# Kernel tuning notes

Measured on AMD Instinct MI355X. Metric: run time of the kernel, lower is better.

The kernel has to match this reference:

```python
import jax, jax.numpy as jnp
import numpy as np

N_NODES = 100000
N_EDGES = 1_600_000
D_IN = 128
D_OUT = 128


def setup_inputs() -> dict:
    key = jax.random.key(0)
    k1, k2, k3 = jax.random.split(key, 3)
    input_matrix = jax.random.normal(k1, (N_NODES, D_IN), dtype=jnp.float32)
    adjacency_coo_matrix = jax.random.randint(k2, (2, N_EDGES), 0, N_NODES, dtype=jnp.int64)
    # xavier-uniform-style init for the weight matrix
    limit = float(np.sqrt(6.0 / (D_IN + D_OUT)))
    weights_matrix = jax.random.uniform(k3, (D_IN, D_OUT), dtype=jnp.float32, minval=-limit, maxval=limit)
    return {
        "input_matrix": input_matrix,
        "adjacency_coo_matrix": adjacency_coo_matrix,
        "weights_matrix": weights_matrix,
    }


def reference(input_matrix, adjacency_coo_matrix, weights_matrix):
    # Edge-wise gathers (the irregular-access pattern from the torch code)
    src_idx = adjacency_coo_matrix[0]
    dst_idx = adjacency_coo_matrix[1]
    neighbors = input_matrix[dst_idx]  # [E, D_IN] gather of neighbor features
    # Mean-aggregate neighbor features onto each src node
    agg = jax.ops.segment_sum(neighbors, src_idx, num_segments=N_NODES)  # [N, D_IN]
    deg = jax.ops.segment_sum(jnp.ones((neighbors.shape[0],), dtype=input_matrix.dtype),
                              src_idx, num_segments=N_NODES)  # [N]
    mean_agg = agg / jnp.maximum(deg, 1.0)[:, None]
    # Linear transform with the layer weight matrix
    out = mean_agg @ weights_matrix  # [N, D_OUT]
    return out
```

## Files before the change

### kernel.cpp

```cpp
#include <hip/hip_runtime.h>

#define NN 100000
#define NE 1600000
#define DD 128
#define CAP 64
#define SLICE_N 12500
#define FILL_BLOCKS 1024
#define BPS (FILL_BLOCKS / 8)
#define GEMM_ROWS 128
#define GEMM_BLOCKS ((NN + GEMM_ROWS - 1) / GEMM_ROWS)

typedef __bf16 bf16x8 __attribute__((ext_vector_type(8)));
typedef float  f32x4  __attribute__((ext_vector_type(4)));

__device__ __forceinline__ unsigned int f2bf(float f) {
    unsigned int u = __float_as_uint(f);
    return (u + 0x7FFFu + ((u >> 16) & 1u)) >> 16;
}
__device__ __forceinline__ float bflo(unsigned int u) { return __uint_as_float(u << 16); }
__device__ __forceinline__ float bfhi(unsigned int u) { return __uint_as_float(u & 0xFFFF0000u); }

__global__ __launch_bounds__(256) void k_prep(const float* __restrict__ W,
                                              unsigned short* __restrict__ wtb,
                                              int* __restrict__ cnt)
{
    const int idx = blockIdx.x * 256 + (int)threadIdx.x;
    const int k = idx >> 7, n = idx & 127;
    wtb[n * DD + k] = (unsigned short)f2bf(W[idx]);
    int4* c4 = (int4*)cnt;
    for (int i = idx; i < NN / 4; i += DD * DD) c4[i] = make_int4(0, 0, 0, 0);
}

__global__ __launch_bounds__(256, 8) void k_fused(const int* __restrict__ adj,
                                                  int* __restrict__ cnt,
                                                  int* __restrict__ edge_dst,
                                                  const float* __restrict__ x,
                                                  const unsigned short* __restrict__ wtb,
                                                  unsigned short* __restrict__ y)
{
    if (blockIdx.x < FILL_BLOCKS) {
        const int slice = blockIdx.x & 7;
        const int w     = blockIdx.x >> 3;
        const int lo    = slice * SLICE_N;
        const uint4* src4 = (const uint4*)adj;
        const uint4* dst4 = (const uint4*)(adj + NE);
        const int ngroups = NE / 4;
        const int stride  = BPS * 256;

        #define PROC(s4, d4) do {                                                     \
            _Pragma("unroll")                                                         \
            for (int j = 0; j < 4; ++j) {                                             \
                const int s = (j==0)?(int)(s4).x:(j==1)?(int)(s4).y:                  \
                              (j==2)?(int)(s4).z:(int)(s4).w;                         \
                const int d = (j==0)?(int)(d4).x:(j==1)?(int)(d4).y:                  \
                              (j==2)?(int)(d4).z:(int)(d4).w;                         \
                if ((unsigned)(s - lo) < (unsigned)SLICE_N) {                         \
                    int slot = atomicAdd(&cnt[s], 1);                                 \
                    if (slot < CAP) edge_dst[(size_t)s * CAP + slot] = d;             \
                }                                                                     \
            }                                                                         \
        } while (0)

        int g = w * 256 + (int)threadIdx.x;
        for (; g + stride < ngroups; g += 2 * stride) {
            const uint4 sa = src4[g],          da = dst4[g];
            const uint4 sb = src4[g + stride], db = dst4[g + stride];
            PROC(sa, da);
            PROC(sb, db);
        }
        for (; g < ngroups; g += stride) {
            const uint4 s4 = src4[g], d4 = dst4[g];
            PROC(s4, d4);
        }
        #undef PROC
        return;
    }

    const int bid  = blockIdx.x - FILL_BLOCKS;
    const int wave = (int)threadIdx.x >> 6;
    const int lane = (int)threadIdx.x & 63;
    const int quad = lane >> 4;
    const int l16  = lane & 15;

    #pragma unroll 1
    for (int mt = 0; mt < 2; ++mt) {
        const int mbase = bid * GEMM_ROWS + wave * 32 + mt * 16;
        const int m = mbase + l16;

        bf16x8 a[4];
        if (m < NN) {
            const float* arow = x + (size_t)m * DD + quad * 8;
            #pragma unroll
            for (int ks = 0; ks < 4; ++ks) {
                const float4 f0 = *(const float4*)(arow + ks * 32);
                const float4 f1 = *(const float4*)(arow + ks * 32 + 4);
                uint4 p;
                p.x = f2bf(f0.x) | (f2bf(f0.y) << 16);
                p.y = f2bf(f0.z) | (f2bf(f0.w) << 16);
                p.z = f2bf(f1.x) | (f2bf(f1.y) << 16);
                p.w = f2bf(f1.z) | (f2bf(f1.w) << 16);
                a[ks] = __builtin_bit_cast(bf16x8, p);
            }
        } else {
            const uint4 z = make_uint4(0, 0, 0, 0);
            #pragma unroll
            for (int ks = 0; ks < 4; ++ks) a[ks] = __builtin_bit_cast(bf16x8, z);
        }

        #pragma unroll
        for (int nt = 0; nt < 8; ++nt) {
            f32x4 c = {0.f, 0.f, 0.f, 0.f};
            const unsigned short* bcol = wtb + (nt * 16 + l16) * DD + quad * 8;
            #pragma unroll
            for (int ks = 0; ks < 4; ++ks) {
                const bf16x8 b = __builtin_bit_cast(bf16x8, *(const uint4*)(bcol + ks * 32));
                c = __builtin_amdgcn_mfma_f32_16x16x32_bf16(a[ks], b, c, 0, 0, 0);
            }
            #pragma unroll
            for (int r = 0; r < 4; ++r) {
                const int row = mbase + quad * 4 + r;
                if (row < NN)
                    y[(size_t)row * DD + nt * 16 + l16] = (unsigned short)f2bf(c[r]);
            }
        }
    }
}

__global__ __launch_bounds__(256) void k_agg2(const unsigned short* __restrict__ y,
                                              const int* __restrict__ cnt,
                                              const int* __restrict__ edge_dst,
                                              float* __restrict__ out)
{
    const int n    = blockIdx.x * 4 + ((int)threadIdx.x >> 6);
    const int lane = (int)threadIdx.x & 63;
    const int eg   = lane >> 4;
    const int h    = lane & 15;
    int deg = cnt[n];
    if (deg > CAP) deg = CAP;
    const int* el = edge_dst + (size_t)n * CAP;

    float acc[8] = {0.f,0.f,0.f,0.f,0.f,0.f,0.f,0.f};

    #define ACC(p) do {                                         \
        acc[0] += bflo((p).x); acc[1] += bfhi((p).x);           \
        acc[2] += bflo((p).y); acc[3] += bfhi((p).y);           \
        acc[4] += bflo((p).z); acc[5] += bfhi((p).z);           \
        acc[6] += bflo((p).w); acc[7] += bfhi((p).w);           \
    } while (0)

    int i = eg;
    for (; i + 12 < deg; i += 16) {
        const int d0 = el[i];
        const int d1 = el[i + 4];
        const int d2 = el[i + 8];
        const int d3 = el[i + 12];
        const uint4 p0 = *(const uint4*)(y + (size_t)d0 * DD + h * 8);
        const uint4 p1 = *(const uint4*)(y + (size_t)d1 * DD + h * 8);
        const uint4 p2 = *(const uint4*)(y + (size_t)d2 * DD + h * 8);
        const uint4 p3 = *(const uint4*)(y + (size_t)d3 * DD + h * 8);
        ACC(p0); ACC(p1); ACC(p2); ACC(p3);
    }
    for (; i + 4 < deg; i += 8) {
        const int d0 = el[i];
        const int d1 = el[i + 4];
        const uint4 p0 = *(const uint4*)(y + (size_t)d0 * DD + h * 8);
        const uint4 p1 = *(const uint4*)(y + (size_t)d1 * DD + h * 8);
        ACC(p0); ACC(p1);
    }
    for (; i < deg; i += 4) {
        const int d0 = el[i];
        const uint4 p0 = *(const uint4*)(y + (size_t)d0 * DD + h * 8);
        ACC(p0);
    }
    #undef ACC

    #pragma unroll
    for (int j = 0; j < 8; ++j) {
        acc[j] += __shfl_xor(acc[j], 16, 64);
        acc[j] += __shfl_xor(acc[j], 32, 64);
    }

    if (eg == 0) {
        const float inv = 1.0f / fmaxf((float)deg, 1.0f);
        float* o = out + (size_t)n * DD + h * 8;
        float4 w0 = {acc[0]*inv, acc[1]*inv, acc[2]*inv, acc[3]*inv};
        float4 w1 = {acc[4]*inv, acc[5]*inv, acc[6]*inv, acc[7]*inv};
        *(float4*)(o + 0) = w0;
        *(float4*)(o + 4) = w1;
    }
}

extern "C" void kernel_launch(void* const* d_in, const int* in_sizes, int n_in,
                              void* d_out, int out_size, void* d_ws, size_t ws_size,
                              hipStream_t stream) {
    const float* x   = (const float*)d_in[0];
    const int*   adj = (const int*)d_in[1];
    const float* W   = (const float*)d_in[2];
    float* out = (float*)d_out;

    unsigned short* y   = (unsigned short*)d_ws;
    unsigned short* wtb = y + (size_t)NN * DD;
    int* cnt      = (int*)(wtb + DD * DD);
    int* edge_dst = cnt + NN;

    k_prep <<<DD * DD / 256, 256, 0, stream>>>(W, wtb, cnt);
    k_fused<<<FILL_BLOCKS + GEMM_BLOCKS, 256, 0, stream>>>(adj, cnt, edge_dst, x, wtb, y);
    k_agg2 <<<NN / 4, 256, 0, stream>>>(y, cnt, edge_dst, out);
}
```

Before: 303.7 us.

## Stage GEMM output through LDS and fold GEMM into fill blocks

The fused kernel now runs the same blocks for both jobs: every block first does its slice of the CSR-bucket fill, and the first 1563 blocks then compute a 64-row bf16 GEMM tile. GEMM results go into a padded LDS tile and are written to global memory as coalesced 16-byte row stores, replacing the scattered 2-byte stores. The fill loop issues all four atomics before the edge_dst stores so their latencies overlap, and fill blocks are doubled to 2048. The risk is that GEMM work now waits behind the atomic-bound fill inside each block, where before it ran in separate concurrent blocks.

```diff
diff --git a/kernel.cpp b/kernel.cpp
--- a/kernel.cpp
+++ b/kernel.cpp
@@ -5,10 +5,10 @@
 #define DD 128
 #define CAP 64
 #define SLICE_N 12500
-#define FILL_BLOCKS 1024
+#define FILL_BLOCKS 2048
 #define BPS (FILL_BLOCKS / 8)
-#define GEMM_ROWS 128
-#define GEMM_BLOCKS ((NN + GEMM_ROWS - 1) / GEMM_ROWS)
+#define GEMM_BLOCKS ((NN + 63) / 64)
+#define LDSP 136
 
 typedef __bf16 bf16x8 __attribute__((ext_vector_type(8)));
 typedef float  f32x4  __attribute__((ext_vector_type(4)));
@@ -38,92 +38,102 @@
                                                   const unsigned short* __restrict__ wtb,
                                                   unsigned short* __restrict__ y)
 {
-    if (blockIdx.x < FILL_BLOCKS) {
-        const int slice = blockIdx.x & 7;
-        const int w     = blockIdx.x >> 3;
+    __shared__ unsigned short ytile[64 * LDSP];
+
+    const int b = blockIdx.x;
+
+    {
+        const int slice = b & 7;
+        const int w     = b >> 3;
         const int lo    = slice * SLICE_N;
         const uint4* src4 = (const uint4*)adj;
         const uint4* dst4 = (const uint4*)(adj + NE);
         const int ngroups = NE / 4;
         const int stride  = BPS * 256;
 
-        #define PROC(s4, d4) do {                                                     \
-            _Pragma("unroll")                                                         \
-            for (int j = 0; j < 4; ++j) {                                             \
-                const int s = (j==0)?(int)(s4).x:(j==1)?(int)(s4).y:                  \
-                              (j==2)?(int)(s4).z:(int)(s4).w;                         \
-                const int d = (j==0)?(int)(d4).x:(j==1)?(int)(d4).y:                  \
-                              (j==2)?(int)(d4).z:(int)(d4).w;                         \
-                if ((unsigned)(s - lo) < (unsigned)SLICE_N) {                         \
-                    int slot = atomicAdd(&cnt[s], 1);                                 \
-                    if (slot < CAP) edge_dst[(size_t)s * CAP + slot] = d;             \
-                }                                                                     \
-            }                                                                         \
-        } while (0)
-
-        int g = w * 256 + (int)threadIdx.x;
-        for (; g + stride < ngroups; g += 2 * stride) {
-            const uint4 sa = src4[g],          da = dst4[g];
-            const uint4 sb = src4[g + stride], db = dst4[g + stride];
-            PROC(sa, da);
-            PROC(sb, db);
+        for (int g = w * 256 + (int)threadIdx.x; g < ngroups; g += stride) {
+            const uint4 s4 = src4[g];
+            const uint4 d4 = dst4[g];
+            const int sv[4] = {(int)s4.x, (int)s4.y, (int)s4.z, (int)s4.w};
+            const int dv[4] = {(int)d4.x, (int)d4.y, (int)d4.z, (int)d4.w};
+            int slot[4];
+            #pragma unroll
+            for (int j = 0; j < 4; ++j) {
+                slot[j] = ((unsigned)(sv[j] - lo) < (unsigned)SLICE_N)
+                          ? atomicAdd(&cnt[sv[j]], 1) : CAP;
+            }
+            #pragma unroll
+            for (int j = 0; j < 4; ++j) {
+                if (slot[j] < CAP)
+                    edge_dst[(size_t)sv[j] * CAP + slot[j]] = dv[j];
+            }
         }
-        for (; g < ngroups; g += stride) {
-            const uint4 s4 = src4[g], d4 = dst4[g];
-            PROC(s4, d4);
-        }
-        #undef PROC
-        return;
-    }
-
-    const int bid  = blockIdx.x - FILL_BLOCKS;
+    }
+
+    if (b >= GEMM_BLOCKS) return;
+
     const int wave = (int)threadIdx.x >> 6;
     const int lane = (int)threadIdx.x & 63;
     const int quad = lane >> 4;
     const int l16  = lane & 15;
-
-    #pragma unroll 1
-    for (int mt = 0; mt < 2; ++mt) {
-        const int mbase = bid * GEMM_ROWS + wave * 32 + mt * 16;
-        const int m = mbase + l16;
-
-        bf16x8 a[4];
-        if (m < NN) {
-            const float* arow = x + (size_t)m * DD + quad * 8;
-            #pragma unroll
-            for (int ks = 0; ks < 4; ++ks) {
-                const float4 f0 = *(const float4*)(arow + ks * 32);
-                const float4 f1 = *(const float4*)(arow + ks * 32 + 4);
-                uint4 p;
-                p.x = f2bf(f0.x) | (f2bf(f0.y) << 16);
-                p.y = f2bf(f0.z) | (f2bf(f0.w) << 16);
-                p.z = f2bf(f1.x) | (f2bf(f1.y) << 16);
-                p.w = f2bf(f1.z) | (f2bf(f1.w) << 16);
-                a[ks] = __builtin_bit_cast(bf16x8, p);
-            }
-        } else {
-            const uint4 z = make_uint4(0, 0, 0, 0);
-            #pragma unroll
-            for (int ks = 0; ks < 4; ++ks) a[ks] = __builtin_bit_cast(bf16x8, z);
+    const int mbase = b * 64 + wave * 16;
+    const int m = mbase + l16;
+
+    bf16x8 a[4];
+    if (m < NN) {
+        const float* arow = x + (size_t)m * DD + quad * 8;
+        #pragma unroll
+        for (int ks = 0; ks < 4; ++ks) {
+            const float4 f0 = *(const float4*)(arow + ks * 32);
+            const float4 f1 = *(const float4*)(arow + ks * 32 + 4);
+            uint4 p;
+            p.x = f2bf(f0.x) | (f2bf(f0.y) << 16);
+            p.y = f2bf(f0.z) | (f2bf(f0.w) << 16);
+            p.z = f2bf(f1.x) | (f2bf(f1.y) << 16);
+            p.w = f2bf(f1.z) | (f2bf(f1.w) << 16);
+            a[ks] = __builtin_bit_cast(bf16x8, p);
         }
-
-        #pragma unroll
-        for (int nt = 0; nt < 8; ++nt) {
-            f32x4 c = {0.f, 0.f, 0.f, 0.f};
-            const unsigned short* bcol = wtb + (nt * 16 + l16) * DD + quad * 8;
-            #pragma unroll
-            for (int ks = 0; ks < 4; ++ks) {
-                const bf16x8 b = __builtin_bit_cast(bf16x8, *(const uint4*)(bcol + ks * 32));
-                c = __builtin_amdgcn_mfma_f32_16x16x32_bf16(a[ks], b, c, 0, 0, 0);
-            }
-            #pragma unroll
-            for (int r = 0; r < 4; ++r) {
-                const int row = mbase + quad * 4 + r;
-                if (row < NN)
-                    y[(size_t)row * DD + nt * 16 + l16] = (unsigned short)f2bf(c[r]);
-            }
+    } else {
+        const uint4 z = make_uint4(0, 0, 0, 0);
+        #pragma unroll
+        for (int ks = 0; ks < 4; ++ks) a[ks] = __builtin_bit_cast(bf16x8, z);
+    }
+
+    unsigned short* lrow = ytile + wave * 16 * LDSP;
+
+    #pragma unroll
+    for (int nt = 0; nt < 8; ++nt) {
+        f32x4 c = {0.f, 0.f, 0.f, 0.f};
+        const unsigned short* bcol = wtb + (nt * 16 + l16) * DD + quad * 8;
+        #pragma unroll
+        for (int ks = 0; ks < 4; ++ks) {
+            const bf16x8 bb = __builtin_bit_cast(bf16x8, *(const uint4*)(bcol + ks * 32));
+            c = __builtin_amdgcn_mfma_f32_16x16x32_bf16(a[ks], bb, c, 0, 0, 0);
         }
-    }
+        #pragma unroll
+        for (int r = 0; r < 4; ++r)
+            lrow[(quad * 4 + r) * LDSP + nt * 16 + l16] = (unsigned short)f2bf(c[r]);
+    }
+
+    __syncthreads();
+
+    const int r16  = lane >> 2;
+    const int ch   = lane & 3;
+    const int grow = mbase - l16 + ( (lane >> 2) );
+    const int growr = b * 64 + wave * 16 + r16;
+    if (growr < NN) {
+        const unsigned short* lsrc = ytile + (wave * 16 + r16) * LDSP + ch * 32;
+        unsigned short* gdst = y + (size_t)growr * DD + ch * 32;
+        const uint4 q0 = *(const uint4*)(lsrc + 0);
+        const uint4 q1 = *(const uint4*)(lsrc + 8);
+        const uint4 q2 = *(const uint4*)(lsrc + 16);
+        const uint4 q3 = *(const uint4*)(lsrc + 24);
+        *(uint4*)(gdst + 0)  = q0;
+        *(uint4*)(gdst + 8)  = q1;
+        *(uint4*)(gdst + 16) = q2;
+        *(uint4*)(gdst + 24) = q3;
+    }
+    (void)grow; (void)r16;
 }
 
 __global__ __launch_bounds__(256) void k_agg2(const unsigned short* __restrict__ y,
@@ -204,6 +214,6 @@
     int* edge_dst = cnt + NN;
 
     k_prep <<<DD * DD / 256, 256, 0, stream>>>(W, wtb, cnt);
-    k_fused<<<FILL_BLOCKS + GEMM_BLOCKS, 256, 0, stream>>>(adj, cnt, edge_dst, x, wtb, y);
+    k_fused<<<FILL_BLOCKS, 256, 0, stream>>>(adj, cnt, edge_dst, x, wtb, y);
     k_agg2 <<<NN / 4, 256, 0, stream>>>(y, cnt, edge_dst, out);
 }
```

After: 252.2 us. 1.2x faster.
